# Kernel optimization log

Measured on AMD Instinct MI355X. Metric: run time of the kernel, lower is better.

Reference implementation:

```python
import jax, jax.numpy as jnp
import numpy as np

B, N, D = 128, 512, 256
NUM_TYPES, NUM_STATS = 6, 8
W_TYPE, W_STATS, W_CORR = 1.0, 1.0, 0.5
LN_EPS = 1e-5


def _mlp_head(x, W1, b1, g, be, W2, b2):
    # Linear -> GELU(exact) -> LayerNorm -> Linear (dropout is identity in eval)
    h = x @ W1 + b1
    h = jax.nn.gelu(h, approximate=False)
    mu = jnp.mean(h, axis=-1, keepdims=True)
    var = jnp.var(h, axis=-1, keepdims=True)
    h = (h - mu) / jnp.sqrt(var + LN_EPS) * g + be
    return h @ W2 + b2


def _masked_mean(x, m):
    m = m.astype(x.dtype)
    return jnp.sum(x * m) / jnp.maximum(jnp.sum(m), 1.0)


def setup_inputs() -> dict:
    key = jax.random.key(0)
    ks = jax.random.split(key, 16)
    s = 1.0 / np.sqrt(D)
    return {
        'column_embeddings': jax.random.normal(ks[0], (B, N, D), jnp.float32),
        'masked_columns': jax.random.uniform(ks[1], (B, N)) < 0.15,
        'type_targets': jax.random.randint(ks[2], (B, N), 0, NUM_TYPES),
        'column_statistics': jax.random.normal(ks[3], (B, N, NUM_STATS), jnp.float32),
        'column_correlations': jax.random.normal(ks[4], (B, N, N), jnp.float32),
        # type head params
        'Wt1': jax.random.normal(ks[5], (D, D), jnp.float32) * s,
        'bt1': jnp.zeros((D,), jnp.float32),
        'gt': jnp.ones((D,), jnp.float32),
        'blt': jnp.zeros((D,), jnp.float32),
        'Wt2': jax.random.normal(ks[6], (D, NUM_TYPES), jnp.float32) * s,
        'bt2': jnp.zeros((NUM_TYPES,), jnp.float32),
        # stats head params
        'Ws1': jax.random.normal(ks[7], (D, D), jnp.float32) * s,
        'bs1': jnp.zeros((D,), jnp.float32),
        'gs': jnp.ones((D,), jnp.float32),
        'bls': jnp.zeros((D,), jnp.float32),
        'Ws2': jax.random.normal(ks[8], (D, NUM_STATS), jnp.float32) * s,
        'bs2': jnp.zeros((NUM_STATS,), jnp.float32),
        # bilinear correlation head (nn.Bilinear(d,d,1) weight [1,d,d] -> [d,d])
        'Wc': jax.random.normal(ks[9], (D, D), jnp.float32) * s,
        'bc': jnp.zeros((), jnp.float32),
    }


def reference(column_embeddings, masked_columns, type_targets, column_statistics,
              column_correlations, Wt1, bt1, gt, blt, Wt2, bt2,
              Ws1, bs1, gs, bls, Ws2, bs2, Wc, bc):
    x = column_embeddings
    m = masked_columns

    type_logits = _mlp_head(x, Wt1, bt1, gt, blt, Wt2, bt2)   # [B,N,6]
    stats_preds = _mlp_head(x, Ws1, bs1, gs, bls, Ws2, bs2)   # [B,N,8]

    # fused bilinear correlation: replaces the O(N^2) python loop
    scores = jnp.einsum('bid,de,bje->bij', x, Wc, x) + bc     # [B,N,N]
    corr = jnp.tanh(scores)
    eye = jnp.eye(N, dtype=bool)
    corr = jnp.where(eye, jnp.ones((), corr.dtype), corr)

    # type loss: masked-mean cross-entropy
    logp = jax.nn.log_softmax(type_logits, axis=-1)
    nll = -jnp.take_along_axis(logp, type_targets[..., None], axis=-1)[..., 0]
    type_loss = _masked_mean(nll, m)

    # stats loss: masked-mean MSE over all stat elements of masked columns
    se = (stats_preds - column_statistics) ** 2
    stats_loss = _masked_mean(se, jnp.broadcast_to(m[:, :, None], se.shape))

    # correlation loss: mask is union over row/col masked columns
    m2 = m[:, :, None] | m[:, None, :]
    corr_loss = _masked_mean((corr - column_correlations) ** 2, m2)

    total = W_TYPE * type_loss + W_STATS * stats_loss + W_CORR * corr_loss
    return total
```

## Files before the change

### kernel.cpp

```cpp
#include <hip/hip_runtime.h>
#include <hip/hip_bf16.h>

#define BB 128
#define NN 512
#define DD 256

typedef __attribute__((ext_vector_type(4))) float f32x4;
typedef __attribute__((ext_vector_type(8))) short s16x8;
typedef __attribute__((ext_vector_type(8))) __bf16 bf16x8;

static __device__ __forceinline__ bf16x8 as_bf(s16x8 v) {
  return __builtin_bit_cast(bf16x8, v);
}

static __device__ __forceinline__ unsigned short f2bf(float f) {
  unsigned u = __builtin_bit_cast(unsigned, f);
  u += 0x7FFFu + ((u >> 16) & 1u);
  return (unsigned short)(u >> 16);
}

static __device__ __forceinline__ float gelu_fast(float h) {
  float z = 1.5957691216057308f * h * (1.0f + 0.044715f * h * h);
  float e = __expf(z);
  float r = __builtin_amdgcn_rcpf(e + 1.0f);
  return h - h * r;
}

__device__ __forceinline__ float wave_sum(float v) {
#pragma unroll
  for (int o = 32; o > 0; o >>= 1) v += __shfl_xor(v, o);
  return v;
}

__global__ void k_init(int* wsi) {
  if (threadIdx.x < 8) wsi[threadIdx.x] = 0;
}

__global__ void k_counts(const int* __restrict__ msk, int* __restrict__ wsi) {
  const int b = blockIdx.x;
  int cnt = 0;
  for (int i = threadIdx.x; i < NN; i += blockDim.x) cnt += (msk[b * NN + i] != 0) ? 1 : 0;
  float s = wave_sum((float)cnt);
  __shared__ float red[4];
  const int lane = threadIdx.x & 63, wv = threadIdx.x >> 6;
  if (lane == 0) red[wv] = s;
  __syncthreads();
  if (threadIdx.x == 0) {
    int k = (int)(red[0] + red[1] + red[2] + red[3] + 0.5f);
    atomicAdd(&wsi[4], k);
    atomicAdd(&wsi[5], NN * NN - (NN - k) * (NN - k));
  }
}

__global__ void k_prep(const float* __restrict__ Wc, const float* __restrict__ Wt1,
                       const float* __restrict__ Ws1, const float* __restrict__ Wt2,
                       const float* __restrict__ Ws2,
                       unsigned short* __restrict__ WcT, unsigned short* __restrict__ Wt1T,
                       unsigned short* __restrict__ Ws1T, unsigned short* __restrict__ Wt2T,
                       unsigned short* __restrict__ Ws2T) {
  int t = blockIdx.x * 256 + threadIdx.x;
  int c = t >> 8, d = t & 255;
  WcT [c * 256 + d] = f2bf(Wc [d * 256 + c]);
  Wt1T[c * 256 + d] = f2bf(Wt1[d * 256 + c]);
  Ws1T[c * 256 + d] = f2bf(Ws1[d * 256 + c]);
  if (c < 16) {
    Wt2T[c * 256 + d] = (c < 6) ? f2bf(Wt2[d * 6 + c]) : (unsigned short)0;
    Ws2T[c * 256 + d] = (c < 8) ? f2bf(Ws2[d * 8 + c]) : (unsigned short)0;
  }
}

__global__ __launch_bounds__(512) void k_heads(
    const float* __restrict__ x, unsigned short* __restrict__ xbf,
    const int* __restrict__ msk,
    const int* __restrict__ tgt, const float* __restrict__ stats,
    const unsigned short* __restrict__ Wt1T, const unsigned short* __restrict__ Ws1T,
    const unsigned short* __restrict__ Wt2T, const unsigned short* __restrict__ Ws2T,
    const float* __restrict__ bt1, const float* __restrict__ bs1,
    const float* __restrict__ gt, const float* __restrict__ gs,
    const float* __restrict__ blt, const float* __restrict__ bls,
    const float* __restrict__ bt2, const float* __restrict__ bs2,
    float* __restrict__ fs)
{
  const int tid = threadIdx.x;
  const int lane = tid & 63, w = tid >> 6;
  const int wm = w & 1, wn = w >> 1;
  const int fr = lane & 15, fg = lane >> 4;
  const int row0 = blockIdx.x * 128;

  __shared__ __align__(16) unsigned short lds_x[128 * 264];
  __shared__ __align__(16) unsigned short pool[33792 + 4224];
  __shared__ float lg[128 * 8];
  unsigned short* lds_h  = pool;
  unsigned short* lds_w2 = pool + 33792;
  float* red = (float*)(pool + 33792);

#pragma unroll
  for (int p = 0; p < 8; ++p) {
    int c = tid + p * 512;
    int r = c >> 5, ch = c & 31;
    const float4* s = (const float4*)&x[(size_t)(row0 + r) * DD + ch * 8];
    float4 v0 = s[0], v1 = s[1];
    uint4 pk;
    pk.x = (unsigned)f2bf(v0.x) | ((unsigned)f2bf(v0.y) << 16);
    pk.y = (unsigned)f2bf(v0.z) | ((unsigned)f2bf(v0.w) << 16);
    pk.z = (unsigned)f2bf(v1.x) | ((unsigned)f2bf(v1.y) << 16);
    pk.w = (unsigned)f2bf(v1.z) | ((unsigned)f2bf(v1.w) << 16);
    *(uint4*)&lds_x[r * 264 + ch * 8] = pk;
    *(uint4*)&xbf[(size_t)(row0 + r) * DD + ch * 8] = pk;
  }
  __syncthreads();

  {
    f32x4 acc[4][4];
#pragma unroll
    for (int i = 0; i < 4; ++i)
#pragma unroll
      for (int j = 0; j < 4; ++j) acc[i][j] = f32x4{0.f, 0.f, 0.f, 0.f};

#pragma unroll
    for (int ks = 0; ks < 8; ++ks) {
      const int ko = ks * 32 + fg * 8;
      s16x8 af[4], bfv[4];
#pragma unroll
      for (int i = 0; i < 4; ++i)
        af[i] = *(const s16x8*)&lds_x[(wm * 64 + i * 16 + fr) * 264 + ko];
#pragma unroll
      for (int j = 0; j < 4; ++j)
        bfv[j] = *(const s16x8*)&Wt1T[(size_t)(wn * 64 + j * 16 + fr) * DD + ko];
#pragma unroll
      for (int i = 0; i < 4; ++i)
#pragma unroll
        for (int j = 0; j < 4; ++j)
          acc[i][j] = __builtin_amdgcn_mfma_f32_16x16x32_bf16(as_bf(af[i]), as_bf(bfv[j]), acc[i][j], 0, 0, 0);
    }

    float sA[16], qA[16];
#pragma unroll
    for (int k = 0; k < 16; ++k) { sA[k] = 0.f; qA[k] = 0.f; }
#pragma unroll
    for (int i = 0; i < 4; ++i)
#pragma unroll
      for (int j = 0; j < 4; ++j) {
        int col = wn * 64 + j * 16 + fr;
        float bb = bt1[col];
#pragma unroll
        for (int r = 0; r < 4; ++r) {
          float h = gelu_fast(acc[i][j][r] + bb);
          acc[i][j][r] = h;
          sA[i * 4 + r] += h;
          qA[i * 4 + r] += h * h;
        }
      }
#pragma unroll
    for (int o = 1; o < 16; o <<= 1) {
#pragma unroll
      for (int k = 0; k < 16; ++k) {
        sA[k] += __shfl_xor(sA[k], o);
        qA[k] += __shfl_xor(qA[k], o);
      }
    }
    if (fr == 0) {
#pragma unroll
      for (int i = 0; i < 4; ++i)
#pragma unroll
        for (int r = 0; r < 4; ++r) {
          int row = wm * 64 + i * 16 + fg * 4 + r;
          red[row * 8 + wn]     = sA[i * 4 + r];
          red[row * 8 + 4 + wn] = qA[i * 4 + r];
        }
    }
    __syncthreads();
#pragma unroll
    for (int i = 0; i < 4; ++i)
#pragma unroll
      for (int r = 0; r < 4; ++r) {
        int row = wm * 64 + i * 16 + fg * 4 + r;
        float s = red[row * 8 + 0] + red[row * 8 + 1] + red[row * 8 + 2] + red[row * 8 + 3];
        float q = red[row * 8 + 4] + red[row * 8 + 5] + red[row * 8 + 6] + red[row * 8 + 7];
        float mu = s * (1.0f / DD);
        float var = q * (1.0f / DD) - mu * mu;
        float rstd = rsqrtf(var + 1e-5f);
#pragma unroll
        for (int j = 0; j < 4; ++j) {
          int col = wn * 64 + j * 16 + fr;
          float hn = (acc[i][j][r] - mu) * rstd * gt[col] + blt[col];
          lds_h[row * 264 + col] = f2bf(hn);
        }
      }
    __syncthreads();
    {
      int r = tid >> 5, ch = tid & 31;
      *(uint4*)&lds_w2[r * 264 + ch * 8] = *(const uint4*)&Wt2T[r * 256 + ch * 8];
    }
    __syncthreads();
    {
      f32x4 a1 = f32x4{0.f, 0.f, 0.f, 0.f};
#pragma unroll
      for (int ks = 0; ks < 8; ++ks) {
        s16x8 av = *(const s16x8*)&lds_h[(w * 16 + fr) * 264 + ks * 32 + fg * 8];
        s16x8 bv = *(const s16x8*)&lds_w2[fr * 264 + ks * 32 + fg * 8];
        a1 = __builtin_amdgcn_mfma_f32_16x16x32_bf16(as_bf(av), as_bf(bv), a1, 0, 0, 0);
      }
      if (fr < 8) {
#pragma unroll
        for (int r = 0; r < 4; ++r) lg[(w * 16 + fg * 4 + r) * 8 + fr] = a1[r];
      }
    }
    __syncthreads();
    if (tid < 128) {
      int grow = row0 + tid;
      int mbit = msk[grow];
      float l[6], mx = -1e30f;
#pragma unroll
      for (int c = 0; c < 6; ++c) { l[c] = lg[tid * 8 + c] + bt2[c]; mx = fmaxf(mx, l[c]); }
      float se = 0.0f;
#pragma unroll
      for (int c = 0; c < 6; ++c) se += expf(l[c] - mx);
      float lse = mx + logf(se);
      int t = tgt[grow];
      float lt = 0.0f;
#pragma unroll
      for (int c = 0; c < 6; ++c) lt = (c == t) ? l[c] : lt;
      float contrib = mbit ? (lse - lt) : 0.0f;
      float s = wave_sum(contrib);
      if ((tid & 63) == 0) atomicAdd(&fs[0], s);
    }
    __syncthreads();
  }

  {
    f32x4 acc[4][4];
#pragma unroll
    for (int i = 0; i < 4; ++i)
#pragma unroll
      for (int j = 0; j < 4; ++j) acc[i][j] = f32x4{0.f, 0.f, 0.f, 0.f};

#pragma unroll
    for (int ks = 0; ks < 8; ++ks) {
      const int ko = ks * 32 + fg * 8;
      s16x8 af[4], bfv[4];
#pragma unroll
      for (int i = 0; i < 4; ++i)
        af[i] = *(const s16x8*)&lds_x[(wm * 64 + i * 16 + fr) * 264 + ko];
#pragma unroll
      for (int j = 0; j < 4; ++j)
        bfv[j] = *(const s16x8*)&Ws1T[(size_t)(wn * 64 + j * 16 + fr) * DD + ko];
#pragma unroll
      for (int i = 0; i < 4; ++i)
#pragma unroll
        for (int j = 0; j < 4; ++j)
          acc[i][j] = __builtin_amdgcn_mfma_f32_16x16x32_bf16(as_bf(af[i]), as_bf(bfv[j]), acc[i][j], 0, 0, 0);
    }

    float sA[16], qA[16];
#pragma unroll
    for (int k = 0; k < 16; ++k) { sA[k] = 0.f; qA[k] = 0.f; }
#pragma unroll
    for (int i = 0; i < 4; ++i)
#pragma unroll
      for (int j = 0; j < 4; ++j) {
        int col = wn * 64 + j * 16 + fr;
        float bb = bs1[col];
#pragma unroll
        for (int r = 0; r < 4; ++r) {
          float h = gelu_fast(acc[i][j][r] + bb);
          acc[i][j][r] = h;
          sA[i * 4 + r] += h;
          qA[i * 4 + r] += h * h;
        }
      }
#pragma unroll
    for (int o = 1; o < 16; o <<= 1) {
#pragma unroll
      for (int k = 0; k < 16; ++k) {
        sA[k] += __shfl_xor(sA[k], o);
        qA[k] += __shfl_xor(qA[k], o);
      }
    }
    if (fr == 0) {
#pragma unroll
      for (int i = 0; i < 4; ++i)
#pragma unroll
        for (int r = 0; r < 4; ++r) {
          int row = wm * 64 + i * 16 + fg * 4 + r;
          red[row * 8 + wn]     = sA[i * 4 + r];
          red[row * 8 + 4 + wn] = qA[i * 4 + r];
        }
    }
    __syncthreads();
#pragma unroll
    for (int i = 0; i < 4; ++i)
#pragma unroll
      for (int r = 0; r < 4; ++r) {
        int row = wm * 64 + i * 16 + fg * 4 + r;
        float s = red[row * 8 + 0] + red[row * 8 + 1] + red[row * 8 + 2] + red[row * 8 + 3];
        float q = red[row * 8 + 4] + red[row * 8 + 5] + red[row * 8 + 6] + red[row * 8 + 7];
        float mu = s * (1.0f / DD);
        float var = q * (1.0f / DD) - mu * mu;
        float rstd = rsqrtf(var + 1e-5f);
#pragma unroll
        for (int j = 0; j < 4; ++j) {
          int col = wn * 64 + j * 16 + fr;
          float hn = (acc[i][j][r] - mu) * rstd * gs[col] + bls[col];
          lds_h[row * 264 + col] = f2bf(hn);
        }
      }
    __syncthreads();
    {
      int r = tid >> 5, ch = tid & 31;
      *(uint4*)&lds_w2[r * 264 + ch * 8] = *(const uint4*)&Ws2T[r * 256 + ch * 8];
    }
    __syncthreads();
    {
      f32x4 a1 = f32x4{0.f, 0.f, 0.f, 0.f};
#pragma unroll
      for (int ks = 0; ks < 8; ++ks) {
        s16x8 av = *(const s16x8*)&lds_h[(w * 16 + fr) * 264 + ks * 32 + fg * 8];
        s16x8 bv = *(const s16x8*)&lds_w2[fr * 264 + ks * 32 + fg * 8];
        a1 = __builtin_amdgcn_mfma_f32_16x16x32_bf16(as_bf(av), as_bf(bv), a1, 0, 0, 0);
      }
      if (fr < 8) {
#pragma unroll
        for (int r = 0; r < 4; ++r) lg[(w * 16 + fg * 4 + r) * 8 + fr] = a1[r];
      }
    }
    __syncthreads();
    if (tid < 128) {
      int grow = row0 + tid;
      int mbit = msk[grow];
      const float* st = stats + (size_t)grow * 8;
      float sse = 0.0f;
#pragma unroll
      for (int c = 0; c < 8; ++c) {
        float d = (lg[tid * 8 + c] + bs2[c]) - st[c];
        sse += d * d;
      }
      float contrib = mbit ? sse : 0.0f;
      float s = wave_sum(contrib);
      if ((tid & 63) == 0) atomicAdd(&fs[1], s);
    }
  }
}

__global__ __launch_bounds__(512) void k_corr(
    const unsigned short* __restrict__ xbf, const int* __restrict__ msk,
    const float* __restrict__ corr, const unsigned short* __restrict__ WcT,
    const float* __restrict__ bcp, float* __restrict__ fs)
{
  const int tid = threadIdx.x;
  const int b  = blockIdx.x >> 3;
  const int it = blockIdx.x & 7;
  const int i0 = it * 64;
  const int lane = tid & 63, w = tid >> 6;
  const int wn = w;
  const int fr = lane & 15, fg = lane >> 4;

  __shared__ __align__(16) unsigned short lds_y[64 * 264];
  __shared__ __align__(16) unsigned short lds_a[64 * 72];
  __shared__ __align__(16) unsigned short lds_b[256 * 72];
  __shared__ int ms_i[64];
  __shared__ int ms_j[256];
  __shared__ float red8[8];

  const unsigned short* xb = xbf + (size_t)b * NN * DD;

  f32x4 acc[4][2];
#pragma unroll
  for (int i = 0; i < 4; ++i)
#pragma unroll
    for (int j = 0; j < 2; ++j) acc[i][j] = f32x4{0.f, 0.f, 0.f, 0.f};

  for (int kt = 0; kt < 4; ++kt) {
    __syncthreads();
    {
      int r = tid >> 3, ch = tid & 7;
      *(uint4*)&lds_a[r * 72 + ch * 8] = *(const uint4*)&xb[(size_t)(i0 + r) * DD + kt * 64 + ch * 8];
    }
#pragma unroll
    for (int p = 0; p < 4; ++p) {
      int idx = tid + p * 512;
      int r = idx >> 3, ch = idx & 7;
      *(uint4*)&lds_b[r * 72 + ch * 8] = *(const uint4*)&WcT[r * 256 + kt * 64 + ch * 8];
    }
    __syncthreads();
#pragma unroll
    for (int ks = 0; ks < 2; ++ks) {
      s16x8 af[4], bfv[2];
#pragma unroll
      for (int i = 0; i < 4; ++i)
        af[i] = *(const s16x8*)&lds_a[(i * 16 + fr) * 72 + ks * 32 + fg * 8];
#pragma unroll
      for (int j = 0; j < 2; ++j)
        bfv[j] = *(const s16x8*)&lds_b[(wn * 32 + j * 16 + fr) * 72 + ks * 32 + fg * 8];
#pragma unroll
      for (int i = 0; i < 4; ++i)
#pragma unroll
        for (int j = 0; j < 2; ++j)
          acc[i][j] = __builtin_amdgcn_mfma_f32_16x16x32_bf16(as_bf(af[i]), as_bf(bfv[j]), acc[i][j], 0, 0, 0);
    }
  }
#pragma unroll
  for (int i = 0; i < 4; ++i)
#pragma unroll
    for (int j = 0; j < 2; ++j)
#pragma unroll
      for (int r = 0; r < 4; ++r) {
        int row = i * 16 + fg * 4 + r;
        int col = wn * 32 + j * 16 + fr;
        lds_y[row * 264 + col] = f2bf(acc[i][j][r]);
      }
  if (tid < 64) ms_i[tid] = msk[b * NN + i0 + tid];

  const float bc = bcp[0];
  const float* tb = corr + (size_t)b * NN * NN;
  float sse = 0.0f;

  for (int jc = 0; jc < 2; ++jc) {
    const int j0 = jc * 256;
#pragma unroll
    for (int i = 0; i < 4; ++i)
#pragma unroll
      for (int j = 0; j < 2; ++j) acc[i][j] = f32x4{0.f, 0.f, 0.f, 0.f};

    for (int kt = 0; kt < 4; ++kt) {
      __syncthreads();
#pragma unroll
      for (int p = 0; p < 4; ++p) {
        int idx = tid + p * 512;
        int r = idx >> 3, ch = idx & 7;
        *(uint4*)&lds_b[r * 72 + ch * 8] = *(const uint4*)&xb[(size_t)(j0 + r) * DD + kt * 64 + ch * 8];
      }
      if (kt == 0 && tid < 256) ms_j[tid] = msk[b * NN + j0 + tid];
      __syncthreads();
#pragma unroll
      for (int ks = 0; ks < 2; ++ks) {
        s16x8 af[4], bfv[2];
#pragma unroll
        for (int i = 0; i < 4; ++i)
          af[i] = *(const s16x8*)&lds_y[(i * 16 + fr) * 264 + kt * 64 + ks * 32 + fg * 8];
#pragma unroll
        for (int j = 0; j < 2; ++j)
          bfv[j] = *(const s16x8*)&lds_b[(wn * 32 + j * 16 + fr) * 72 + ks * 32 + fg * 8];
#pragma unroll
        for (int i = 0; i < 4; ++i)
#pragma unroll
          for (int j = 0; j < 2; ++j)
            acc[i][j] = __builtin_amdgcn_mfma_f32_16x16x32_bf16(as_bf(af[i]), as_bf(bfv[j]), acc[i][j], 0, 0, 0);
      }
    }

    float tg[4][2][4];
#pragma unroll
    for (int i = 0; i < 4; ++i) {
      int rbase = i0 + i * 16 + fg * 4;
#pragma unroll
      for (int j = 0; j < 2; ++j) {
        int gj = j0 + wn * 32 + j * 16 + fr;
#pragma unroll
        for (int r = 0; r < 4; ++r)
          tg[i][j][r] = tb[(size_t)(rbase + r) * NN + gj];
      }
    }

#pragma unroll
    for (int i = 0; i < 4; ++i) {
      int rbase = i * 16 + fg * 4;
#pragma unroll
      for (int j = 0; j < 2; ++j) {
        int colc = wn * 32 + j * 16 + fr;
        int gj = j0 + colc;
        int mj = ms_j[colc];
#pragma unroll
        for (int r = 0; r < 4; ++r) {
          int gi = i0 + rbase + r;
          float s = acc[i][j][r] + bc;
          float e = __expf(2.0f * s);
          float cv = 1.0f - 2.0f * __builtin_amdgcn_rcpf(e + 1.0f);
          if (gi == gj) cv = 1.0f;
          float d = cv - tg[i][j][r];
          int mb = ms_i[rbase + r] | mj;
          sse += mb ? d * d : 0.0f;
        }
      }
    }
  }

  float s = wave_sum(sse);
  if (lane == 0) red8[w] = s;
  __syncthreads();
  if (tid == 0) {
    float t = 0.f;
#pragma unroll
    for (int i = 0; i < 8; ++i) t += red8[i];
    atomicAdd(&fs[2], t);
  }
}

__global__ void k_final(const float* __restrict__ fs, const int* __restrict__ wsi,
                        float* __restrict__ out) {
  if (threadIdx.x == 0 && blockIdx.x == 0) {
    float cm = (float)wsi[4];
    float c2 = (float)wsi[5];
    out[0] = fs[0] / fmaxf(cm, 1.0f) + fs[1] / fmaxf(8.0f * cm, 1.0f) +
             0.5f * fs[2] / fmaxf(c2, 1.0f);
  }
}

extern "C" void kernel_launch(void* const* d_in, const int* in_sizes, int n_in,
                              void* d_out, int out_size, void* d_ws, size_t ws_size,
                              hipStream_t stream) {
  const float* x     = (const float*)d_in[0];
  const int*   msk   = (const int*)d_in[1];
  const int*   tgt   = (const int*)d_in[2];
  const float* stats = (const float*)d_in[3];
  const float* corr  = (const float*)d_in[4];
  const float* Wt1   = (const float*)d_in[5];
  const float* bt1   = (const float*)d_in[6];
  const float* gt    = (const float*)d_in[7];
  const float* blt   = (const float*)d_in[8];
  const float* Wt2   = (const float*)d_in[9];
  const float* bt2   = (const float*)d_in[10];
  const float* Ws1   = (const float*)d_in[11];
  const float* bs1   = (const float*)d_in[12];
  const float* gs    = (const float*)d_in[13];
  const float* bls   = (const float*)d_in[14];
  const float* Ws2   = (const float*)d_in[15];
  const float* bs2   = (const float*)d_in[16];
  const float* Wc    = (const float*)d_in[17];
  const float* bc    = (const float*)d_in[18];

  float* fs = (float*)d_ws;
  int* wsi  = (int*)d_ws;
  unsigned short* WcT  = (unsigned short*)((char*)d_ws + 256);
  unsigned short* Wt1T = WcT + 65536;
  unsigned short* Ws1T = Wt1T + 65536;
  unsigned short* Wt2T = Ws1T + 65536;
  unsigned short* Ws2T = Wt2T + 4096;
  unsigned short* xbf  = Ws2T + 4096;

  hipLaunchKernelGGL(k_init, dim3(1), dim3(64), 0, stream, wsi);
  hipLaunchKernelGGL(k_counts, dim3(BB), dim3(256), 0, stream, msk, wsi);
  hipLaunchKernelGGL(k_prep, dim3(256), dim3(256), 0, stream,
                     Wc, Wt1, Ws1, Wt2, Ws2, WcT, Wt1T, Ws1T, Wt2T, Ws2T);
  hipLaunchKernelGGL(k_heads, dim3((BB * NN) / 128), dim3(512), 0, stream,
                     x, xbf, msk, tgt, stats, Wt1T, Ws1T, Wt2T, Ws2T,
                     bt1, bs1, gt, gs, blt, bls, bt2, bs2, fs);
  hipLaunchKernelGGL(k_corr, dim3(BB * (NN / 64)), dim3(512), 0, stream,
                     xbf, msk, corr, WcT, bc, fs);
  hipLaunchKernelGGL(k_final, dim3(1), dim3(64), 0, stream, fs, wsi, (float*)d_out);
}
```

Baseline: 176.0 us.

## Compute both head first-layer GEMMs in one pass and alias hidden buffer onto x tile

Both heads' first-layer GEMMs now run in a single k-loop that shares the A-fragment loads from the x tile in LDS. With x no longer needed afterward, the hidden activation buffer is aliased onto the x LDS tile, which shrinks shared memory per block by about 67 KB. The cost is holding two 4x4 accumulator sets live at once (128 extra VGPRs), which can increase register pressure or cause spills. The smaller LDS footprint may allow more blocks per CU.

```diff
diff --git a/kernel.cpp b/kernel.cpp
--- a/kernel.cpp
+++ b/kernel.cpp
@@ -88,11 +88,11 @@
   const int row0 = blockIdx.x * 128;
 
   __shared__ __align__(16) unsigned short lds_x[128 * 264];
-  __shared__ __align__(16) unsigned short pool[33792 + 4224];
+  __shared__ __align__(16) unsigned short pool2[4224];
   __shared__ float lg[128 * 8];
-  unsigned short* lds_h  = pool;
-  unsigned short* lds_w2 = pool + 33792;
-  float* red = (float*)(pool + 33792);
+  unsigned short* lds_h  = lds_x;
+  unsigned short* lds_w2 = pool2;
+  float* red = (float*)pool2;
 
 #pragma unroll
   for (int p = 0; p < 8; ++p) {
@@ -110,30 +110,37 @@
   }
   __syncthreads();
 
+  f32x4 at[4][4], asx[4][4];
+#pragma unroll
+  for (int i = 0; i < 4; ++i)
+#pragma unroll
+    for (int j = 0; j < 4; ++j) {
+      at[i][j]  = f32x4{0.f, 0.f, 0.f, 0.f};
+      asx[i][j] = f32x4{0.f, 0.f, 0.f, 0.f};
+    }
+
+#pragma unroll
+  for (int ks = 0; ks < 8; ++ks) {
+    const int ko = ks * 32 + fg * 8;
+    s16x8 af[4], bt_[4], bs_[4];
+#pragma unroll
+    for (int i = 0; i < 4; ++i)
+      af[i] = *(const s16x8*)&lds_x[(wm * 64 + i * 16 + fr) * 264 + ko];
+#pragma unroll
+    for (int j = 0; j < 4; ++j) {
+      bt_[j] = *(const s16x8*)&Wt1T[(size_t)(wn * 64 + j * 16 + fr) * DD + ko];
+      bs_[j] = *(const s16x8*)&Ws1T[(size_t)(wn * 64 + j * 16 + fr) * DD + ko];
+    }
+#pragma unroll
+    for (int i = 0; i < 4; ++i)
+#pragma unroll
+      for (int j = 0; j < 4; ++j) {
+        at[i][j]  = __builtin_amdgcn_mfma_f32_16x16x32_bf16(as_bf(af[i]), as_bf(bt_[j]), at[i][j], 0, 0, 0);
+        asx[i][j] = __builtin_amdgcn_mfma_f32_16x16x32_bf16(as_bf(af[i]), as_bf(bs_[j]), asx[i][j], 0, 0, 0);
+      }
+  }
+
   {
-    f32x4 acc[4][4];
-#pragma unroll
-    for (int i = 0; i < 4; ++i)
-#pragma unroll
-      for (int j = 0; j < 4; ++j) acc[i][j] = f32x4{0.f, 0.f, 0.f, 0.f};
-
-#pragma unroll
-    for (int ks = 0; ks < 8; ++ks) {
-      const int ko = ks * 32 + fg * 8;
-      s16x8 af[4], bfv[4];
-#pragma unroll
-      for (int i = 0; i < 4; ++i)
-        af[i] = *(const s16x8*)&lds_x[(wm * 64 + i * 16 + fr) * 264 + ko];
-#pragma unroll
-      for (int j = 0; j < 4; ++j)
-        bfv[j] = *(const s16x8*)&Wt1T[(size_t)(wn * 64 + j * 16 + fr) * DD + ko];
-#pragma unroll
-      for (int i = 0; i < 4; ++i)
-#pragma unroll
-        for (int j = 0; j < 4; ++j)
-          acc[i][j] = __builtin_amdgcn_mfma_f32_16x16x32_bf16(as_bf(af[i]), as_bf(bfv[j]), acc[i][j], 0, 0, 0);
-    }
-
     float sA[16], qA[16];
 #pragma unroll
     for (int k = 0; k < 16; ++k) { sA[k] = 0.f; qA[k] = 0.f; }
@@ -145,8 +152,8 @@
         float bb = bt1[col];
 #pragma unroll
         for (int r = 0; r < 4; ++r) {
-          float h = gelu_fast(acc[i][j][r] + bb);
-          acc[i][j][r] = h;
+          float h = gelu_fast(at[i][j][r] + bb);
+          at[i][j][r] = h;
           sA[i * 4 + r] += h;
           qA[i * 4 + r] += h * h;
         }
@@ -183,7 +190,7 @@
 #pragma unroll
         for (int j = 0; j < 4; ++j) {
           int col = wn * 64 + j * 16 + fr;
-          float hn = (acc[i][j][r] - mu) * rstd * gt[col] + blt[col];
+          float hn = (at[i][j][r] - mu) * rstd * gt[col] + blt[col];
           lds_h[row * 264 + col] = f2bf(hn);
         }
       }
@@ -229,29 +236,6 @@
   }
 
   {
-    f32x4 acc[4][4];
-#pragma unroll
-    for (int i = 0; i < 4; ++i)
-#pragma unroll
-      for (int j = 0; j < 4; ++j) acc[i][j] = f32x4{0.f, 0.f, 0.f, 0.f};
-
-#pragma unroll
-    for (int ks = 0; ks < 8; ++ks) {
-      const int ko = ks * 32 + fg * 8;
-      s16x8 af[4], bfv[4];
-#pragma unroll
-      for (int i = 0; i < 4; ++i)
-        af[i] = *(const s16x8*)&lds_x[(wm * 64 + i * 16 + fr) * 264 + ko];
-#pragma unroll
-      for (int j = 0; j < 4; ++j)
-        bfv[j] = *(const s16x8*)&Ws1T[(size_t)(wn * 64 + j * 16 + fr) * DD + ko];
-#pragma unroll
-      for (int i = 0; i < 4; ++i)
-#pragma unroll
-        for (int j = 0; j < 4; ++j)
-          acc[i][j] = __builtin_amdgcn_mfma_f32_16x16x32_bf16(as_bf(af[i]), as_bf(bfv[j]), acc[i][j], 0, 0, 0);
-    }
-
     float sA[16], qA[16];
 #pragma unroll
     for (int k = 0; k < 16; ++k) { sA[k] = 0.f; qA[k] = 0.f; }
@@ -263,8 +247,8 @@
         float bb = bs1[col];
 #pragma unroll
         for (int r = 0; r < 4; ++r) {
-          float h = gelu_fast(acc[i][j][r] + bb);
-          acc[i][j][r] = h;
+          float h = gelu_fast(asx[i][j][r] + bb);
+          asx[i][j][r] = h;
           sA[i * 4 + r] += h;
           qA[i * 4 + r] += h * h;
         }
@@ -301,7 +285,7 @@
 #pragma unroll
         for (int j = 0; j < 4; ++j) {
           int col = wn * 64 + j * 16 + fr;
-          float hn = (acc[i][j][r] - mu) * rstd * gs[col] + bls[col];
+          float hn = (asx[i][j][r] - mu) * rstd * gs[col] + bls[col];
           lds_h[row * 264 + col] = f2bf(hn);
         }
       }
```

After: 172.9 us (median of 3 runs). No clear change (-1.7%).
